# Kernel optimization log

Measured on AMD Instinct MI355X. Metric: run time of the kernel, lower is better.

Reference implementation:

```python
import jax, jax.numpy as jnp
import numpy as np

B, T, N, FI, FO = 4, 8, 1024, 64, 64
ALPHA = 0.2          # LeakyReLU negative slope
NEG_INF = -1e12      # matches torch's -1000000000000.0


def setup_inputs() -> dict:
    key = jax.random.key(0)
    k0, k1, k2, k3, k4 = jax.random.split(key, 5)
    inp = jax.random.normal(k0, (B, T, N, FI), dtype=jnp.float32)
    u = jax.random.uniform(k1, (T, N, N), dtype=jnp.float32)
    adj = jnp.where(u > 0.9, u, 0.0)
    # att_mask: [batch, node, seq] in {0,1}
    att_mask = (jax.random.uniform(k2, (B, N, T)) > 0.2).astype(jnp.float32)
    # xavier-ish init (gain 1.414)
    W = jax.random.normal(k3, (FI, FO), dtype=jnp.float32) * (1.414 * np.sqrt(2.0 / (FI + FO)))
    a = jax.random.normal(k4, (2 * FO, 1), dtype=jnp.float32) * (1.414 * np.sqrt(2.0 / (2 * FO + 1)))
    return {"adj": adj, "inp": inp, "att_mask": att_mask, "W": W, "a": a}


def reference(adj, inp, att_mask, W, a):
    Fo = W.shape[1]
    h = jnp.einsum('btnf,fo->btno', inp, W)               # [B,T,N,Fo]
    # additive decomposition of a^T [h_i || h_j] = a1.h_i + a2.h_j
    a1 = a[:Fo, 0]
    a2 = a[Fo:, 0]
    s1 = jnp.einsum('btno,o->btn', h, a1)                 # contributes along rows (i)
    s2 = jnp.einsum('btno,o->btn', h, a2)                 # contributes along cols (j)
    e = s1[..., :, None] + s2[..., None, :]               # [B,T,N,N]
    e = jnp.where(e > 0, e, ALPHA * e)                    # LeakyReLU
    att = jnp.where(adj > 0, e * adj, NEG_INF)            # adj broadcasts over batch
    att = jax.nn.softmax(att, axis=-1)
    m = jnp.transpose(att_mask, (0, 2, 1))                # [B,T,N]
    att = att * (m[..., :, None] * m[..., None, :])       # outer-product mask
    # dropout is identity in eval mode
    h_prime = jnp.einsum('btij,btjo->btio', att, h)       # [B,T,N,Fo]
    return jax.nn.elu(h_prime)                            # concat=True path
```

## Files before the change

kernel.cpp:

```cpp
#include <hip/hip_runtime.h>
#include <hip/hip_bf16.h>
#include <math.h>

#define N_NODES 1024
#define T_DIM 8

typedef __bf16 bf16x8 __attribute__((ext_vector_type(8)));
typedef float  f32x4  __attribute__((ext_vector_type(4)));

__device__ __forceinline__ float readlane_f(float v, int l) {
    return __uint_as_float(__builtin_amdgcn_readlane(__float_as_uint(v), l));
}

__global__ __launch_bounds__(256) void gat_h_kernel(
    const float* __restrict__ inp, const float* __restrict__ W,
    const float* __restrict__ a, const float* __restrict__ att_mask,
    const float* __restrict__ adj, float* __restrict__ adjT,
    __bf16* __restrict__ hF, float* __restrict__ s1w, float* __restrict__ s2w)
{
    __shared__ float Wl[64 * 64];
    __shared__ float xl[64 * 64];
    __shared__ __bf16 htl[64 * 72];

    const int tid  = threadIdx.x;
    const int blk  = blockIdx.x;
    const int bt   = blk >> 4;
    const int b    = bt >> 3;
    const int t    = bt & 7;
    const int nt   = blk & 15;
    const int n0   = nt * 64;
    const int lane = tid & 63;
    const int wave = tid >> 6;

    const float4* W4  = (const float4*)W;
    float4*       Wl4 = (float4*)Wl;
    const float4* x4  = (const float4*)(inp + (size_t)(bt * N_NODES + n0) * 64);
    float4*       xl4 = (float4*)xl;
#pragma unroll
    for (int k = 0; k < 4; ++k) {
        Wl4[tid + k * 256] = W4[tid + k * 256];
        xl4[tid + k * 256] = x4[tid + k * 256];
    }
    const float a1 = a[lane];
    const float a2 = a[64 + lane];
    __syncthreads();

#pragma unroll 1
    for (int rg = 0; rg < 16; rg += 4) {
        float xr[4], acc[4];
#pragma unroll
        for (int q = 0; q < 4; ++q) {
            xr[q]  = xl[(wave * 16 + rg + q) * 64 + lane];
            acc[q] = 0.f;
        }
#pragma unroll
        for (int f = 0; f < 64; ++f) {
            float w = Wl[f * 64 + lane];
#pragma unroll
            for (int q = 0; q < 4; ++q)
                acc[q] = fmaf(readlane_f(xr[q], f), w, acc[q]);
        }
#pragma unroll
        for (int q = 0; q < 4; ++q) {
            const int r = wave * 16 + rg + q;
            float v1 = acc[q] * a1, v2 = acc[q] * a2;
#pragma unroll
            for (int off = 32; off; off >>= 1) {
                v1 += __shfl_xor(v1, off, 64);
                v2 += __shfl_xor(v2, off, 64);
            }
            if (lane == 0) {
                s1w[bt * N_NODES + n0 + r] = v1;
                s2w[bt * N_NODES + n0 + r] = v2;
            }
            const float mjr = att_mask[((size_t)b * N_NODES + n0 + r) * T_DIM + t];
            htl[lane * 72 + r] = (__bf16)(acc[q] * mjr);
        }
    }
    __syncthreads();

    {
        const int l  = tid & 63;
        const int w  = tid >> 6;
        __bf16* tbase = hF + (size_t)(bt * 16 + nt) * 4096;
#pragma unroll
        for (int cc = 0; cc < 2; ++cc) {
            const int c  = w + cc * 4;
            const int nc = c & 3;
            const int kc = c >> 2;
            bf16x8 v = *(const bf16x8*)&htl[(nc * 16 + (l & 15)) * 72
                                            + (l >> 4) * 8 + kc * 32];
            *(bf16x8*)(tbase + (c * 64 + l) * 8) = v;
        }
    }

    {
        const int itile = b * 16 + nt;
        const float* src = adj + (size_t)t * N_NODES * N_NODES
                               + (size_t)(itile * 16 + (lane & 15)) * N_NODES
                               + (lane >> 4) * 8;
        float* dst = adjT + (size_t)(t * 64 + itile) * 16 * 1024 + lane * 16;
#pragma unroll
        for (int jj = 0; jj < 4; ++jj) {
            const int jt = wave + jj * 4;
            f32x4 v0 = *(const f32x4*)(src + jt * 64);
            f32x4 v1 = *(const f32x4*)(src + jt * 64 + 4);
            f32x4 v2 = *(const f32x4*)(src + jt * 64 + 32);
            f32x4 v3 = *(const f32x4*)(src + jt * 64 + 36);
            f32x4* d = (f32x4*)(dst + (size_t)jt * 1024);
            d[0] = v0; d[1] = v1; d[2] = v2; d[3] = v3;
        }
    }
}

__global__ __launch_bounds__(64) void gat_attn_kernel(
    const float* __restrict__ adjT, const float* __restrict__ att_mask,
    const __bf16* __restrict__ hF, const float* __restrict__ s1w,
    const float* __restrict__ s2w, float* __restrict__ out)
{
    const int bt    = blockIdx.y;
    const int b     = bt >> 3;
    const int t     = bt & 7;
    const int itile = blockIdx.x;
    const int irow0 = itile * 16;
    const int lane  = threadIdx.x;
    const int l15   = lane & 15;
    const int quad  = lane >> 4;
    const int phase = itile & 15;

    f32x4 acc[4];
#pragma unroll
    for (int nc = 0; nc < 4; ++nc) acc[nc] = (f32x4){0.f, 0.f, 0.f, 0.f};
    float lsum = 0.f;
    const float s1r = s1w[bt * N_NODES + irow0 + l15];

    const float*  atb = adjT + (size_t)(t * 64 + itile) * 16 * 1024 + lane * 16;
    const __bf16* htb = hF + (size_t)bt * 16 * 4096 + lane * 8;
    const float*  s2p = s2w + bt * N_NODES + quad * 8;

    f32x4  adjc[4];
    f32x4  s2c[4];
    bf16x8 hc[8];
    {
        const int jt = phase;
        const float* ap = atb + (size_t)jt * 1024;
#pragma unroll
        for (int k = 0; k < 4; ++k) adjc[k] = *(const f32x4*)(ap + k * 4);
#pragma unroll
        for (int k = 0; k < 2; ++k) {
            s2c[k]     = *(const f32x4*)(s2p + jt * 64 + k * 4);
            s2c[2 + k] = *(const f32x4*)(s2p + jt * 64 + 32 + k * 4);
        }
        const __bf16* hp = htb + (size_t)jt * 4096;
#pragma unroll
        for (int c = 0; c < 8; ++c) hc[c] = *(const bf16x8*)(hp + c * 512);
    }

#pragma unroll 2
    for (int it = 0; it < 16; ++it) {
        const int jn = (it + 1 + phase) & 15;

        f32x4  adjn[4], s2n[4];
        bf16x8 hn[8];
        {
            const float* ap = atb + (size_t)jn * 1024;
#pragma unroll
            for (int k = 0; k < 4; ++k) adjn[k] = *(const f32x4*)(ap + k * 4);
#pragma unroll
            for (int k = 0; k < 2; ++k) {
                s2n[k]     = *(const f32x4*)(s2p + jn * 64 + k * 4);
                s2n[2 + k] = *(const f32x4*)(s2p + jn * 64 + 32 + k * 4);
            }
            const __bf16* hp = htb + (size_t)jn * 4096;
#pragma unroll
            for (int c = 0; c < 8; ++c) hn[c] = *(const bf16x8*)(hp + c * 512);
        }

        const float* ac = (const float*)adjc;
        const float* sc = (const float*)s2c;
        bf16x8 af[2];
#pragma unroll
        for (int kc = 0; kc < 2; ++kc)
#pragma unroll
            for (int m = 0; m < 8; ++m) {
                float av = ac[kc * 8 + m];
                float e  = s1r + sc[kc * 8 + m];
                e = fmaxf(e, 0.2f * e);
                float p = (av > 0.f) ? __expf(e * av) : 0.f;
                lsum += p;
                af[kc][m] = (__bf16)p;
            }

#pragma unroll
        for (int nc = 0; nc < 4; ++nc)
            acc[nc] = __builtin_amdgcn_mfma_f32_16x16x32_bf16(af[0], hc[nc], acc[nc], 0, 0, 0);
#pragma unroll
        for (int nc = 0; nc < 4; ++nc)
            acc[nc] = __builtin_amdgcn_mfma_f32_16x16x32_bf16(af[1], hc[4 + nc], acc[nc], 0, 0, 0);

#pragma unroll
        for (int k = 0; k < 4; ++k) { adjc[k] = adjn[k]; s2c[k] = s2n[k]; }
#pragma unroll
        for (int c = 0; c < 8; ++c) hc[c] = hn[c];
    }

    lsum += __shfl_xor(lsum, 16, 64);
    lsum += __shfl_xor(lsum, 32, 64);

#pragma unroll
    for (int reg = 0; reg < 4; ++reg) {
        const int i = irow0 + quad * 4 + reg;
        float ls = __shfl(lsum, quad * 4 + reg, 64);
        float mi = att_mask[((size_t)b * N_NODES + i) * T_DIM + t];
        float scale = mi / ls;
#pragma unroll
        for (int nc = 0; nc < 4; ++nc) {
            float v = acc[nc][reg] * scale;
            v = (v > 0.f) ? v : (__expf(v) - 1.f);
            out[((size_t)bt * N_NODES + i) * 64 + nc * 16 + l15] = v;
        }
    }
}

extern "C" void kernel_launch(void* const* d_in, const int* in_sizes, int n_in,
                              void* d_out, int out_size, void* d_ws, size_t ws_size,
                              hipStream_t stream) {
    (void)in_sizes; (void)n_in; (void)out_size; (void)ws_size;
    const float* adj      = (const float*)d_in[0];
    const float* inp      = (const float*)d_in[1];
    const float* att_mask = (const float*)d_in[2];
    const float* W        = (const float*)d_in[3];
    const float* a        = (const float*)d_in[4];
    float* out = (float*)d_out;

    float*  adjT = (float*)d_ws;
    __bf16* hF   = (__bf16*)((char*)d_ws + (size_t)32 * 1024 * 1024);
    float*  s1w  = (float*)((char*)d_ws + (size_t)36 * 1024 * 1024);
    float*  s2w  = s1w + 32 * N_NODES;

    gat_h_kernel<<<512, 256, 0, stream>>>(inp, W, a, att_mask, adj, adjT, hF, s1w, s2w);
    dim3 grid(64, 32);
    gat_attn_kernel<<<grid, 64, 0, stream>>>(adjT, att_mask, hF, s1w, s2w, out);
}
```

Measured before the change: 141.4 us.

## Split attention j-loop across four waves with partial-sum reduce kernel

The attention kernel now uses 256 threads per block. Each wave handles a quarter of the column tiles and writes partial accumulators and row sums to workspace. A new reduce kernel sums the four partials, normalises, applies the mask and ELU, and writes the output. The adjacency transpose is also rewritten so each thread reads whole contiguous rows, giving coalesced loads. This adds parallelism per row tile and shortens the serial loop, at the cost of an extra launch and extra partial-sum traffic through memory.

Measured after the change: 149.8 us. +5.9%, slower.

```diff
diff --git a/kernel.cpp b/kernel.cpp
--- a/kernel.cpp
+++ b/kernel.cpp
@@ -96,37 +96,39 @@
 
     {
         const int itile = b * 16 + nt;
-        const float* src = adj + (size_t)t * N_NODES * N_NODES
-                               + (size_t)(itile * 16 + (lane & 15)) * N_NODES
-                               + (lane >> 4) * 8;
-        float* dst = adjT + (size_t)(t * 64 + itile) * 16 * 1024 + lane * 16;
-#pragma unroll
-        for (int jj = 0; jj < 4; ++jj) {
-            const int jt = wave + jj * 4;
-            f32x4 v0 = *(const f32x4*)(src + jt * 64);
-            f32x4 v1 = *(const f32x4*)(src + jt * 64 + 4);
-            f32x4 v2 = *(const f32x4*)(src + jt * 64 + 32);
-            f32x4 v3 = *(const f32x4*)(src + jt * 64 + 36);
-            f32x4* d = (f32x4*)(dst + (size_t)jt * 1024);
-            d[0] = v0; d[1] = v1; d[2] = v2; d[3] = v3;
-        }
-    }
-}
-
-__global__ __launch_bounds__(64) void gat_attn_kernel(
-    const float* __restrict__ adjT, const float* __restrict__ att_mask,
-    const __bf16* __restrict__ hF, const float* __restrict__ s1w,
-    const float* __restrict__ s2w, float* __restrict__ out)
+        const int i0    = itile * 16;
+        const float* srcb = adj + (size_t)t * N_NODES * N_NODES + (size_t)i0 * N_NODES;
+        float* dstb = adjT + (size_t)(t * 64 + itile) * 16 * 1024;
+        const int c0   = tid * 4;
+        const int jt   = c0 >> 6;
+        const int j6   = c0 & 63;
+        const int kc   = j6 >> 5;
+        const int quad = (j6 >> 3) & 3;
+        const int m0   = j6 & 7;
+        float* dcol = dstb + (size_t)jt * 1024 + quad * 256 + kc * 8 + m0;
+#pragma unroll
+        for (int r = 0; r < 16; ++r) {
+            f32x4 v = *(const f32x4*)(srcb + (size_t)r * N_NODES + c0);
+            *(f32x4*)(dcol + r * 16) = v;
+        }
+    }
+}
+
+__global__ __launch_bounds__(256) void gat_attn_kernel(
+    const float* __restrict__ adjT, const __bf16* __restrict__ hF,
+    const float* __restrict__ s1w, const float* __restrict__ s2w,
+    float* __restrict__ pacc, float* __restrict__ plsum)
 {
     const int bt    = blockIdx.y;
-    const int b     = bt >> 3;
     const int t     = bt & 7;
     const int itile = blockIdx.x;
     const int irow0 = itile * 16;
-    const int lane  = threadIdx.x;
+    const int tid   = threadIdx.x;
+    const int lane  = tid & 63;
+    const int js    = tid >> 6;
     const int l15   = lane & 15;
     const int quad  = lane >> 4;
-    const int phase = itile & 15;
+    const int phase = itile & 3;
 
     f32x4 acc[4];
 #pragma unroll
@@ -138,11 +140,10 @@
     const __bf16* htb = hF + (size_t)bt * 16 * 4096 + lane * 8;
     const float*  s2p = s2w + bt * N_NODES + quad * 8;
 
-    f32x4  adjc[4];
-    f32x4  s2c[4];
+    f32x4  adjc[4], s2c[4];
     bf16x8 hc[8];
     {
-        const int jt = phase;
+        const int jt = js * 4 + phase;
         const float* ap = atb + (size_t)jt * 1024;
 #pragma unroll
         for (int k = 0; k < 4; ++k) adjc[k] = *(const f32x4*)(ap + k * 4);
@@ -157,8 +158,8 @@
     }
 
 #pragma unroll 2
-    for (int it = 0; it < 16; ++it) {
-        const int jn = (it + 1 + phase) & 15;
+    for (int it = 0; it < 4; ++it) {
+        const int jn = js * 4 + ((it + 1 + phase) & 3);
 
         f32x4  adjn[4], s2n[4];
         bf16x8 hn[8];
@@ -204,22 +205,49 @@
         for (int c = 0; c < 8; ++c) hc[c] = hn[c];
     }
 
+    float* pb = pacc + ((size_t)(bt * 64 + itile) * 4 + js) * 1024;
+#pragma unroll
+    for (int nc = 0; nc < 4; ++nc)
+#pragma unroll
+        for (int reg = 0; reg < 4; ++reg)
+            pb[(quad * 4 + reg) * 64 + nc * 16 + l15] = acc[nc][reg];
+
     lsum += __shfl_xor(lsum, 16, 64);
     lsum += __shfl_xor(lsum, 32, 64);
-
-#pragma unroll
-    for (int reg = 0; reg < 4; ++reg) {
-        const int i = irow0 + quad * 4 + reg;
-        float ls = __shfl(lsum, quad * 4 + reg, 64);
-        float mi = att_mask[((size_t)b * N_NODES + i) * T_DIM + t];
-        float scale = mi / ls;
-#pragma unroll
-        for (int nc = 0; nc < 4; ++nc) {
-            float v = acc[nc][reg] * scale;
-            v = (v > 0.f) ? v : (__expf(v) - 1.f);
-            out[((size_t)bt * N_NODES + i) * 64 + nc * 16 + l15] = v;
-        }
-    }
+    if (lane < 16)
+        plsum[((size_t)(bt * 64 + itile) * 4 + js) * 16 + lane] = lsum;
+}
+
+__global__ __launch_bounds__(256) void gat_reduce_kernel(
+    const float* __restrict__ pacc, const float* __restrict__ plsum,
+    const float* __restrict__ att_mask, float* __restrict__ out)
+{
+    const int itile = blockIdx.x;
+    const int bt    = blockIdx.y;
+    const int b     = bt >> 3;
+    const int t     = bt & 7;
+    const int tid   = threadIdx.x;
+    const int row   = tid >> 4;
+    const int c0    = (tid & 15) * 4;
+
+    const float* pb = pacc + (size_t)(bt * 64 + itile) * 4096;
+    f32x4 v = (f32x4){0.f, 0.f, 0.f, 0.f};
+#pragma unroll
+    for (int js = 0; js < 4; ++js)
+        v += *(const f32x4*)(pb + js * 1024 + row * 64 + c0);
+
+    const float* lb = plsum + (size_t)(bt * 64 + itile) * 64;
+    float ls = lb[row] + lb[16 + row] + lb[32 + row] + lb[48 + row];
+
+    const int i = itile * 16 + row;
+    float mi = att_mask[((size_t)b * N_NODES + i) * T_DIM + t];
+    float scale = mi / ls;
+#pragma unroll
+    for (int k = 0; k < 4; ++k) {
+        float x = v[k] * scale;
+        v[k] = (x > 0.f) ? x : (__expf(x) - 1.f);
+    }
+    *(f32x4*)(out + ((size_t)bt * N_NODES + i) * 64 + c0) = v;
 }
 
 extern "C" void kernel_launch(void* const* d_in, const int* in_sizes, int n_in,
@@ -233,12 +261,15 @@
     const float* a        = (const float*)d_in[4];
     float* out = (float*)d_out;
 
-    float*  adjT = (float*)d_ws;
-    __bf16* hF   = (__bf16*)((char*)d_ws + (size_t)32 * 1024 * 1024);
-    float*  s1w  = (float*)((char*)d_ws + (size_t)36 * 1024 * 1024);
-    float*  s2w  = s1w + 32 * N_NODES;
+    float*  adjT  = (float*)d_ws;
+    __bf16* hF    = (__bf16*)((char*)d_ws + (size_t)32 * 1024 * 1024);
+    float*  s1w   = (float*)((char*)d_ws + (size_t)36 * 1024 * 1024);
+    float*  s2w   = s1w + 32 * N_NODES;
+    float*  pacc  = (float*)((char*)d_ws + (size_t)40 * 1024 * 1024);
+    float*  plsum = (float*)((char*)d_ws + (size_t)72 * 1024 * 1024);
 
     gat_h_kernel<<<512, 256, 0, stream>>>(inp, W, a, att_mask, adj, adjT, hF, s1w, s2w);
     dim3 grid(64, 32);
-    gat_attn_kernel<<<grid, 64, 0, stream>>>(adjT, att_mask, hF, s1w, s2w, out);
-}
+    gat_attn_kernel<<<grid, 256, 0, stream>>>(adjT, hF, s1w, s2w, pacc, plsum);
+    gat_reduce_kernel<<<grid, 256, 0, stream>>>(pacc, plsum, att_mask, out);
+}
```
